# Kernel tuning notes

Measured on AMD Instinct MI355X. Metric: run time of the kernel, lower is better.

The kernel has to match this reference:

```python
import jax, jax.numpy as jnp
import numpy as np


def setup_inputs() -> dict:
    key = jax.random.key(0)
    k1, k2, k3, k4 = jax.random.split(key, 4)
    B, H, W, D, C = 1, 20, 20, 20, 64
    x = jax.random.normal(k1, (B, H, W, D, C), dtype=jnp.float32)
    Wb = jax.random.normal(k2, (C, C // 8), dtype=jnp.float32) * 0.05
    Wc = jax.random.normal(k3, (C, C // 8), dtype=jnp.float32) * 0.05
    Wd = jax.random.normal(k4, (C, C), dtype=jnp.float32) * 0.05
    gamma = jnp.zeros((1,), dtype=jnp.float32) + 0.5  # nonzero so attention branch matters
    return {"x": x, "Wb": Wb, "Wc": Wc, "Wd": Wd, "gamma": gamma}


def reference(x, Wb, Wc, Wd, gamma):
    B, H, W, D, C = x.shape
    N = H * W * D
    xf = x.reshape(B, N, C)                       # [B, N, C]
    # 1x1x1 convs (no bias) == per-token dense projections
    b = xf @ Wb                                   # keys    [B, N, C//8]
    c = xf @ Wc                                   # queries [B, N, C//8]
    v = xf @ Wd                                   # values  [B, N, C]
    # scores[i, j] = c_i . b_j  (no 1/sqrt(dk) scaling, matching original)
    scores = jnp.einsum('bnk,bmk->bnm', c, b)     # [B, N, N]
    attn = jax.nn.softmax(scores, axis=-1)
    ctx = jnp.einsum('bnm,bmc->bnc', attn, v)     # [B, N, C]
    out = gamma * ctx + xf
    return out.reshape(B, H, W, D, C)
```

## Files before the change

### kernel.cpp

```cpp
#include <hip/hip_runtime.h>
#include <hip/hip_bf16.h>

typedef __attribute__((ext_vector_type(8))) short short8;
typedef __attribute__((ext_vector_type(16))) float f32x16;
typedef __attribute__((ext_vector_type(4))) float fx4;
typedef __attribute__((ext_vector_type(4))) unsigned uint4v;

#define LOG2E_F 1.4426950408889634f

#define KB_OFF   0u
#define CQ_OFF   65536u
#define ZERO_OFF 130048u
#define VF_OFF   131072u
#define PLS_F    524288u
#define PACC_U   1048576u

__device__ __forceinline__ float fast_exp2(float v) {
#if __has_builtin(__builtin_amdgcn_exp2f)
    return __builtin_amdgcn_exp2f(v);
#else
    return exp2f(v);
#endif
}

__device__ __forceinline__ unsigned short f2bfu(float f) {
    unsigned short u;
    __hip_bfloat16 h = __float2bfloat16(f);
    __builtin_memcpy(&u, &h, 2);
    return u;
}

__device__ __forceinline__ unsigned pk2(float lo, float hi) {
    return (unsigned)f2bfu(lo) | ((unsigned)f2bfu(hi) << 16);
}

__device__ __forceinline__ unsigned pkt(float lo, float hi) {
#if __has_builtin(__builtin_amdgcn_perm)
    return __builtin_amdgcn_perm(__builtin_bit_cast(unsigned, hi),
                                 __builtin_bit_cast(unsigned, lo),
                                 0x07060302u);
#else
    return (__builtin_bit_cast(unsigned, lo) >> 16) |
           (__builtin_bit_cast(unsigned, hi) & 0xffff0000u);
#endif
}

__device__ __forceinline__ short8 cvt8(fx4 a, fx4 b) {
    uint4v u;
    u[0] = pk2(a[0], a[1]);
    u[1] = pk2(a[2], a[3]);
    u[2] = pk2(b[0], b[1]);
    u[3] = pk2(b[2], b[3]);
    return __builtin_bit_cast(short8, u);
}

__global__ __launch_bounds__(128, 1) void pam_proj(
    const float* __restrict__ x,
    const float* __restrict__ Wb,
    const float* __restrict__ Wc,
    const float* __restrict__ Wd,
    unsigned short* __restrict__ ws)
{
    __shared__ alignas(16) unsigned short Wt[96][72];

    const int tid = threadIdx.x;
    if (tid < 8) ws[ZERO_OFF + tid] = 0;
#pragma unroll
    for (int i = 0; i < 32; ++i) {
        int e = i * 128 + tid;
        int col = e & 63, k = e >> 6;
        Wt[16 + col][k] = f2bfu(Wd[k * 64 + col]);
    }
#pragma unroll
    for (int i = 0; i < 8; ++i) {
        int e = i * 128 + tid;
        int c = e & 15, k = e >> 4;
        float w = (c < 8) ? Wb[k * 8 + c] : Wc[k * 8 + (c - 8)] * LOG2E_F;
        Wt[c][k] = f2bfu(w);
    }
#pragma unroll
    for (int i = 0; i < 9; ++i) {
        int e = i * 128 + tid;
        if (e < 1152) Wt[80 + e / 72][e - (e / 72) * 72] = 0;
    }
    __syncthreads();

    const int wave = tid >> 6, lane = tid & 63;
    const int l31 = lane & 31, g = lane >> 5;
    const int rowbase = blockIdx.x * 64 + wave * 32;

    short8 bfrag[3][4];
#pragma unroll
    for (int ct = 0; ct < 3; ++ct)
#pragma unroll
        for (int kk = 0; kk < 4; ++kk)
            bfrag[ct][kk] = *reinterpret_cast<const short8*>(&Wt[ct * 32 + l31][kk * 16 + g * 8]);

    const float* xr = x + (size_t)(rowbase + l31) * 64 + g * 8;
    short8 afrag[4];
#pragma unroll
    for (int kk = 0; kk < 4; ++kk) {
        fx4 a = *reinterpret_cast<const fx4*>(xr + kk * 16);
        fx4 b = *reinterpret_cast<const fx4*>(xr + kk * 16 + 4);
        afrag[kk] = cvt8(a, b);
    }

    f32x16 acc[3] = {};
#pragma unroll
    for (int kk = 0; kk < 4; ++kk)
#pragma unroll
        for (int ct = 0; ct < 3; ++ct)
            acc[ct] = __builtin_amdgcn_mfma_f32_32x32x16_bf16(afrag[kk], bfrag[ct][kk], acc[ct], 0, 0, 0);

#pragma unroll
    for (int ct = 0; ct < 3; ++ct) {
        const int col = ct * 32 + l31;
#pragma unroll
        for (int r = 0; r < 16; ++r) {
            const int row = rowbase + (r & 3) + 8 * (r >> 2) + 4 * g;
            const unsigned short hv = f2bfu(acc[ct][r]);
            if (col < 8) {
                ws[KB_OFF + row * 8u + col] = hv;
            } else if (col < 16) {
                ws[CQ_OFF + row * 8u + (col - 8)] = hv;
            } else if (col < 80) {
                const unsigned j  = col - 16;
                const unsigned t5 = row & 31u;
                const unsigned ks = t5 >> 4;
                const unsigned rr = t5 & 15u;
                const unsigned gg = (rr >> 2) & 1u;
                const unsigned ee = (rr & 3u) + ((rr >> 3) << 2);
                ws[VF_OFF + (row >> 5) * 2048u + ks * 1024u + gg * 512u + j * 8u + ee] = hv;
            }
        }
    }
}

__global__ __launch_bounds__(256, 4) void pam_attn(
    const unsigned short* __restrict__ ws,
    float* __restrict__ wsf,
    unsigned* __restrict__ wsu)
{
    __shared__ alignas(16) unsigned accp[4][32][36];
    __shared__ float ls_s[4][2][32];

    const int tid  = threadIdx.x;
    const int wave = tid >> 6;
    const int lane = tid & 63;
    const int l31  = lane & 31;
    const int g    = lane >> 5;
    const int qt   = blockIdx.x >> 3;
    const int kp   = blockIdx.x & 7;
    const int qbase = qt * 32;

    const short8* cqp = reinterpret_cast<const short8*>(ws + CQ_OFF);
    const short8* vp8 = reinterpret_cast<const short8*>(ws + VF_OFF);

    const unsigned short* kbz = ws + ((lane < 32) ? (KB_OFF + (unsigned)l31 * 8u)
                                                  : ZERO_OFF);
    const unsigned kstep = (lane < 32) ? 256u : 0u;

    short8 cf = {};
    if (lane < 32) cf = cqp[qbase + l31];

    f32x16 acc0 = {}, acc1 = {};
    float ls0 = 0.f, ls1 = 0.f, ls2 = 0.f, ls3 = 0.f;

    const int plen   = (kp < 2) ? 32 : 31;
    const int pstart = kp * 31 + ((kp < 2) ? kp : 2);
    const int s0 = pstart + (plen * wave) / 4;
    const int s1 = pstart + (plen * (wave + 1)) / 4;

    short8 kf = *reinterpret_cast<const short8*>(kbz + (unsigned)s0 * kstep);
    const int vb0 = s0 * 256 + g * 64 + l31;
    short8 v00 = vp8[vb0];
    short8 v01 = vp8[vb0 + 32];
    short8 v10 = vp8[vb0 + 128];
    short8 v11 = vp8[vb0 + 160];

    const f32x16 z = {};
    f32x16 st = __builtin_amdgcn_mfma_f32_32x32x16_bf16(kf, cf, z, 0, 0, 0);

    for (int s = s0; s < s1; ++s) {
        const int sc = (s + 1 < s1) ? (s + 1) : (s1 - 1);
        const short8 kfn = *reinterpret_cast<const short8*>(kbz + (unsigned)sc * kstep);
        const int nb = sc * 256 + g * 64 + l31;
        const short8 n00 = vp8[nb];
        const short8 n01 = vp8[nb + 32];
        const short8 n10 = vp8[nb + 128];
        const short8 n11 = vp8[nb + 160];

        float e[16];
#pragma unroll
        for (int r = 0; r < 16; ++r) e[r] = fast_exp2(st[r]);

        ls0 += (e[0]  + e[1])  + (e[2]  + e[3]);
        ls1 += (e[4]  + e[5])  + (e[6]  + e[7]);
        ls2 += (e[8]  + e[9])  + (e[10] + e[11]);
        ls3 += (e[12] + e[13]) + (e[14] + e[15]);

        uint4v u0, u1;
#pragma unroll
        for (int p = 0; p < 4; ++p) u0[p] = pkt(e[2 * p], e[2 * p + 1]);
#pragma unroll
        for (int p = 0; p < 4; ++p) u1[p] = pkt(e[8 + 2 * p], e[9 + 2 * p]);
        const short8 af0 = __builtin_bit_cast(short8, u0);
        const short8 af1 = __builtin_bit_cast(short8, u1);

        st = __builtin_amdgcn_mfma_f32_32x32x16_bf16(kfn, cf, z, 0, 0, 0);

        acc0 = __builtin_amdgcn_mfma_f32_32x32x16_bf16(af0, v00, acc0, 0, 0, 0);
        acc1 = __builtin_amdgcn_mfma_f32_32x32x16_bf16(af0, v01, acc1, 0, 0, 0);
        acc0 = __builtin_amdgcn_mfma_f32_32x32x16_bf16(af1, v10, acc0, 0, 0, 0);
        acc1 = __builtin_amdgcn_mfma_f32_32x32x16_bf16(af1, v11, acc1, 0, 0, 0);

        v00 = n00; v01 = n01; v10 = n10; v11 = n11;
    }

    ls_s[wave][g][l31] = (ls0 + ls1) + (ls2 + ls3);
#pragma unroll
    for (int r = 0; r < 16; ++r) {
        const int row = (r & 3) + 8 * (r >> 2) + 4 * g;
        accp[wave][row][l31] = pk2(acc0[r], acc1[r]);
    }
    __syncthreads();

    if (tid < 32) {
        float s = 0.f;
#pragma unroll
        for (int w = 0; w < 4; ++w) s += ls_s[w][0][tid] + ls_s[w][1][tid];
        wsf[PLS_F + blockIdx.x * 32u + tid] = s;
    }
    const int q = tid >> 3, c0 = (tid & 7) * 4;
    fx4 alo = {}, ahi = {};
#pragma unroll
    for (int w = 0; w < 4; ++w) {
        const uint4v wv = *reinterpret_cast<const uint4v*>(&accp[w][q][c0]);
#pragma unroll
        for (int t = 0; t < 4; ++t) {
            alo[t] += __builtin_bit_cast(float, wv[t] << 16);
            ahi[t] += __builtin_bit_cast(float, wv[t] & 0xffff0000u);
        }
    }
    uint4v u;
#pragma unroll
    for (int t = 0; t < 4; ++t) u[t] = pk2(alo[t], ahi[t]);
    *reinterpret_cast<uint4v*>(wsu + PACC_U + blockIdx.x * 1024u + q * 32u + c0) = u;
}

__global__ __launch_bounds__(256) void pam_merge(
    const float* __restrict__ x,
    const float* __restrict__ gamma_p,
    const float* __restrict__ wsf,
    const unsigned* __restrict__ wsu,
    float* __restrict__ out)
{
    const int tid = threadIdx.x;
    const int qt  = blockIdx.x;
    const int q   = tid >> 3;
    const int c0  = (tid & 7) * 4;

    float lq = 0.f;
#pragma unroll
    for (int kp = 0; kp < 8; ++kp)
        lq += wsf[PLS_F + (unsigned)(qt * 8 + kp) * 32u + q];

    fx4 alo = {}, ahi = {};
#pragma unroll
    for (int kp = 0; kp < 8; ++kp) {
        const uint4v w = *reinterpret_cast<const uint4v*>(
            wsu + PACC_U + (unsigned)(qt * 8 + kp) * 1024u + q * 32u + c0);
#pragma unroll
        for (int t = 0; t < 4; ++t) {
            alo[t] += __builtin_bit_cast(float, w[t] << 16);
            ahi[t] += __builtin_bit_cast(float, w[t] & 0xffff0000u);
        }
    }

    const float sc = gamma_p[0] / lq;
    const int base = (qt * 32 + q) * 64;

    const fx4 x0 = *reinterpret_cast<const fx4*>(x + base + c0);
    const fx4 x1 = *reinterpret_cast<const fx4*>(x + base + 32 + c0);
    fx4 o0, o1;
#pragma unroll
    for (int t = 0; t < 4; ++t) {
        o0[t] = alo[t] * sc + x0[t];
        o1[t] = ahi[t] * sc + x1[t];
    }
    *reinterpret_cast<fx4*>(out + base + c0)      = o0;
    *reinterpret_cast<fx4*>(out + base + 32 + c0) = o1;
}

extern "C" void kernel_launch(void* const* d_in, const int* in_sizes, int n_in,
                              void* d_out, int out_size, void* d_ws, size_t ws_size,
                              hipStream_t stream)
{
    const float* x     = (const float*)d_in[0];
    const float* Wb    = (const float*)d_in[1];
    const float* Wc    = (const float*)d_in[2];
    const float* Wd    = (const float*)d_in[3];
    const float* gamma = (const float*)d_in[4];
    float* outp = (float*)d_out;
    unsigned short* ws = (unsigned short*)d_ws;
    float* wsf = (float*)d_ws;
    unsigned* wsu = (unsigned*)d_ws;

    hipLaunchKernelGGL(pam_proj, dim3(125), dim3(128), 0, stream, x, Wb, Wc, Wd, ws);
    hipLaunchKernelGGL(pam_attn, dim3(2000), dim3(256), 0, stream,
                       (const unsigned short*)ws, wsf, wsu);
    hipLaunchKernelGGL(pam_merge, dim3(250), dim3(256), 0, stream,
                       x, gamma, (const float*)wsf, (const unsigned*)wsu, outp);
}
```

Measured before the change: 32.93 us.

## Share V tiles across four query tiles via double-buffered LDS staging

Each block now gives each of its four waves a different 32-query tile, and all four iterate over the same key partition. V blocks are staged cooperatively into a double-buffered shared-memory buffer, so the four waves read each V tile once from global memory. This removes the earlier split of keys across waves and the cross-wave LDS reduction, and the grid shrinks from 2000 blocks to 504. In exchange the kernel uses 64KB of LDS per block with per-chunk barriers, runs fewer blocks, and wastes work on padded query tiles beyond 250.

```diff
diff --git a/kernel.cpp b/kernel.cpp
--- a/kernel.cpp
+++ b/kernel.cpp
@@ -136,21 +136,21 @@
     }
 }
 
-__global__ __launch_bounds__(256, 4) void pam_attn(
+__global__ __launch_bounds__(256, 2) void pam_attn(
     const unsigned short* __restrict__ ws,
     float* __restrict__ wsf,
     unsigned* __restrict__ wsu)
 {
-    __shared__ alignas(16) unsigned accp[4][32][36];
-    __shared__ float ls_s[4][2][32];
+    __shared__ alignas(16) unsigned short vbuf[2][16384];
 
     const int tid  = threadIdx.x;
     const int wave = tid >> 6;
     const int lane = tid & 63;
     const int l31  = lane & 31;
     const int g    = lane >> 5;
-    const int qt   = blockIdx.x >> 3;
+    const int qg   = blockIdx.x >> 3;
     const int kp   = blockIdx.x & 7;
+    const int qt   = qg * 4 + wave;
     const int qbase = qt * 32;
 
     const short8* cqp = reinterpret_cast<const short8*>(ws + CQ_OFF);
@@ -168,84 +168,96 @@
 
     const int plen   = (kp < 2) ? 32 : 31;
     const int pstart = kp * 31 + ((kp < 2) ? kp : 2);
-    const int s0 = pstart + (plen * wave) / 4;
-    const int s1 = pstart + (plen * (wave + 1)) / 4;
-
-    short8 kf = *reinterpret_cast<const short8*>(kbz + (unsigned)s0 * kstep);
-    const int vb0 = s0 * 256 + g * 64 + l31;
-    short8 v00 = vp8[vb0];
-    short8 v01 = vp8[vb0 + 32];
-    short8 v10 = vp8[vb0 + 128];
-    short8 v11 = vp8[vb0 + 160];
+    const int pend   = pstart + plen;
+
+    const unsigned vlo = ((unsigned)g * 64u + (unsigned)l31) * 8u;
+
+    short8 stg[8];
+#pragma unroll
+    for (int i = 0; i < 8; ++i) {
+        const int si = (pstart + i < pend) ? (pstart + i) : (pend - 1);
+        stg[i] = vp8[si * 256 + tid];
+    }
+#pragma unroll
+    for (int i = 0; i < 8; ++i)
+        *reinterpret_cast<short8*>(&vbuf[0][i * 2048 + tid * 8]) = stg[i];
+
+    short8 kf = *reinterpret_cast<const short8*>(kbz + (unsigned)pstart * kstep);
+    __syncthreads();
 
     const f32x16 z = {};
     f32x16 st = __builtin_amdgcn_mfma_f32_32x32x16_bf16(kf, cf, z, 0, 0, 0);
 
-    for (int s = s0; s < s1; ++s) {
-        const int sc = (s + 1 < s1) ? (s + 1) : (s1 - 1);
-        const short8 kfn = *reinterpret_cast<const short8*>(kbz + (unsigned)sc * kstep);
-        const int nb = sc * 256 + g * 64 + l31;
-        const short8 n00 = vp8[nb];
-        const short8 n01 = vp8[nb + 32];
-        const short8 n10 = vp8[nb + 128];
-        const short8 n11 = vp8[nb + 160];
-
-        float e[16];
-#pragma unroll
-        for (int r = 0; r < 16; ++r) e[r] = fast_exp2(st[r]);
-
-        ls0 += (e[0]  + e[1])  + (e[2]  + e[3]);
-        ls1 += (e[4]  + e[5])  + (e[6]  + e[7]);
-        ls2 += (e[8]  + e[9])  + (e[10] + e[11]);
-        ls3 += (e[12] + e[13]) + (e[14] + e[15]);
-
-        uint4v u0, u1;
-#pragma unroll
-        for (int p = 0; p < 4; ++p) u0[p] = pkt(e[2 * p], e[2 * p + 1]);
-#pragma unroll
-        for (int p = 0; p < 4; ++p) u1[p] = pkt(e[8 + 2 * p], e[9 + 2 * p]);
-        const short8 af0 = __builtin_bit_cast(short8, u0);
-        const short8 af1 = __builtin_bit_cast(short8, u1);
-
-        st = __builtin_amdgcn_mfma_f32_32x32x16_bf16(kfn, cf, z, 0, 0, 0);
-
-        acc0 = __builtin_amdgcn_mfma_f32_32x32x16_bf16(af0, v00, acc0, 0, 0, 0);
-        acc1 = __builtin_amdgcn_mfma_f32_32x32x16_bf16(af0, v01, acc1, 0, 0, 0);
-        acc0 = __builtin_amdgcn_mfma_f32_32x32x16_bf16(af1, v10, acc0, 0, 0, 0);
-        acc1 = __builtin_amdgcn_mfma_f32_32x32x16_bf16(af1, v11, acc1, 0, 0, 0);
-
-        v00 = n00; v01 = n01; v10 = n10; v11 = n11;
-    }
-
-    ls_s[wave][g][l31] = (ls0 + ls1) + (ls2 + ls3);
-#pragma unroll
-    for (int r = 0; r < 16; ++r) {
-        const int row = (r & 3) + 8 * (r >> 2) + 4 * g;
-        accp[wave][row][l31] = pk2(acc0[r], acc1[r]);
-    }
-    __syncthreads();
-
-    if (tid < 32) {
-        float s = 0.f;
-#pragma unroll
-        for (int w = 0; w < 4; ++w) s += ls_s[w][0][tid] + ls_s[w][1][tid];
-        wsf[PLS_F + blockIdx.x * 32u + tid] = s;
-    }
-    const int q = tid >> 3, c0 = (tid & 7) * 4;
-    fx4 alo = {}, ahi = {};
-#pragma unroll
-    for (int w = 0; w < 4; ++w) {
-        const uint4v wv = *reinterpret_cast<const uint4v*>(&accp[w][q][c0]);
-#pragma unroll
-        for (int t = 0; t < 4; ++t) {
-            alo[t] += __builtin_bit_cast(float, wv[t] << 16);
-            ahi[t] += __builtin_bit_cast(float, wv[t] & 0xffff0000u);
-        }
-    }
-    uint4v u;
-#pragma unroll
-    for (int t = 0; t < 4; ++t) u[t] = pk2(alo[t], ahi[t]);
-    *reinterpret_cast<uint4v*>(wsu + PACC_U + blockIdx.x * 1024u + q * 32u + c0) = u;
+    int p = 0;
+    for (int mb = pstart; mb < pend; mb += 8) {
+        const int nbm  = mb + 8;
+        const bool more = nbm < pend;
+
+        if (more) {
+#pragma unroll
+            for (int i = 0; i < 8; ++i) {
+                const int si = (nbm + i < pend) ? (nbm + i) : (pend - 1);
+                stg[i] = vp8[si * 256 + tid];
+            }
+        }
+
+        const int mend = more ? nbm : pend;
+        for (int s = mb; s < mend; ++s) {
+            const int sc = (s + 1 < pend) ? (s + 1) : (pend - 1);
+            const short8 kfn = *reinterpret_cast<const short8*>(kbz + (unsigned)sc * kstep);
+
+            const unsigned short* vb = &vbuf[p][(unsigned)(s - mb) * 2048u + vlo];
+            const short8 v00 = *reinterpret_cast<const short8*>(vb);
+            const short8 v01 = *reinterpret_cast<const short8*>(vb + 256);
+            const short8 v10 = *reinterpret_cast<const short8*>(vb + 1024);
+            const short8 v11 = *reinterpret_cast<const short8*>(vb + 1280);
+
+            float e[16];
+#pragma unroll
+            for (int r = 0; r < 16; ++r) e[r] = fast_exp2(st[r]);
+
+            ls0 += (e[0]  + e[1])  + (e[2]  + e[3]);
+            ls1 += (e[4]  + e[5])  + (e[6]  + e[7]);
+            ls2 += (e[8]  + e[9])  + (e[10] + e[11]);
+            ls3 += (e[12] + e[13]) + (e[14] + e[15]);
+
+            uint4v u0, u1;
+#pragma unroll
+            for (int pp = 0; pp < 4; ++pp) u0[pp] = pkt(e[2 * pp], e[2 * pp + 1]);
+#pragma unroll
+            for (int pp = 0; pp < 4; ++pp) u1[pp] = pkt(e[8 + 2 * pp], e[9 + 2 * pp]);
+            const short8 af0 = __builtin_bit_cast(short8, u0);
+            const short8 af1 = __builtin_bit_cast(short8, u1);
+
+            st = __builtin_amdgcn_mfma_f32_32x32x16_bf16(kfn, cf, z, 0, 0, 0);
+
+            acc0 = __builtin_amdgcn_mfma_f32_32x32x16_bf16(af0, v00, acc0, 0, 0, 0);
+            acc1 = __builtin_amdgcn_mfma_f32_32x32x16_bf16(af0, v01, acc1, 0, 0, 0);
+            acc0 = __builtin_amdgcn_mfma_f32_32x32x16_bf16(af1, v10, acc0, 0, 0, 0);
+            acc1 = __builtin_amdgcn_mfma_f32_32x32x16_bf16(af1, v11, acc1, 0, 0, 0);
+        }
+
+        if (more) {
+#pragma unroll
+            for (int i = 0; i < 8; ++i)
+                *reinterpret_cast<short8*>(&vbuf[p ^ 1][i * 2048 + tid * 8]) = stg[i];
+            __syncthreads();
+            p ^= 1;
+        }
+    }
+
+    float lst = (ls0 + ls1) + (ls2 + ls3);
+    lst += __shfl_xor(lst, 32);
+    if (qt < 250) {
+        const unsigned pw = (unsigned)qt * 8u + (unsigned)kp;
+        if (lane < 32) wsf[PLS_F + pw * 32u + l31] = lst;
+        const unsigned pb = PACC_U + pw * 1024u;
+#pragma unroll
+        for (int r = 0; r < 16; ++r) {
+            const int q0 = (r & 3) + 8 * (r >> 2) + 4 * g;
+            wsu[pb + (unsigned)q0 * 32u + l31] = pk2(acc0[r], acc1[r]);
+        }
+    }
 }
 
 __global__ __launch_bounds__(256) void pam_merge(
@@ -307,7 +319,7 @@
     unsigned* wsu = (unsigned*)d_ws;
 
     hipLaunchKernelGGL(pam_proj, dim3(125), dim3(128), 0, stream, x, Wb, Wc, Wd, ws);
-    hipLaunchKernelGGL(pam_attn, dim3(2000), dim3(256), 0, stream,
+    hipLaunchKernelGGL(pam_attn, dim3(504), dim3(256), 0, stream,
                        (const unsigned short*)ws, wsf, wsu);
     hipLaunchKernelGGL(pam_merge, dim3(250), dim3(256), 0, stream,
                        x, gamma, (const float*)wsf, (const unsigned*)wsu, outp);
```

After: 32.14 us. -2.4%, faster.
